# Performance work log

Hardware: AMD Instinct MI355X
Metric: run time of the kernel (lower is better)

The kernel has to match this reference:

```python
import jax, jax.numpy as jnp
import numpy as np

DIM = 1024
HEADS = 16
HEAD_DIM = DIM // HEADS


def setup_inputs() -> dict:
    key = jax.random.key(0)
    ks = jax.random.split(key, 5)
    B, N = 4, 2048
    x = jax.random.normal(ks[0], (B, N, DIM), dtype=jnp.float32)
    # nn.Linear default init scale ~ 1/sqrt(fan_in)
    s = 1.0 / np.sqrt(DIM)
    W_qkv = jax.random.uniform(ks[1], (DIM, 3 * DIM), minval=-s, maxval=s, dtype=jnp.float32)
    b_qkv = jax.random.uniform(ks[2], (3 * DIM,), minval=-s, maxval=s, dtype=jnp.float32)
    W_proj = jax.random.uniform(ks[3], (DIM, DIM), minval=-s, maxval=s, dtype=jnp.float32)
    b_proj = jax.random.uniform(ks[4], (DIM,), minval=-s, maxval=s, dtype=jnp.float32)
    return {"x": x, "W_qkv": W_qkv, "b_qkv": b_qkv, "W_proj": W_proj, "b_proj": b_proj}


def reference(x, W_qkv, b_qkv, W_proj, b_proj):
    B, N, C = x.shape
    qkv = x @ W_qkv + b_qkv                      # [B, N, 3C]
    qkv = qkv.reshape(B, N, 3, HEADS, HEAD_DIM)
    q = jnp.transpose(qkv[:, :, 0], (0, 2, 1, 3))  # [B, H, N, D]
    k = jnp.transpose(qkv[:, :, 1], (0, 2, 1, 3))
    v = jnp.transpose(qkv[:, :, 2], (0, 2, 1, 3))
    scale = 1.0 / np.sqrt(HEAD_DIM)
    scores = jnp.einsum('bhqd,bhkd->bhqk', q, k) * scale  # [B, H, N, N]
    attn = jax.nn.softmax(scores, axis=-1)
    out = jnp.einsum('bhqk,bhkd->bhqd', attn, v)           # [B, H, N, D]
    out = jnp.transpose(out, (0, 2, 1, 3)).reshape(B, N, C)
    return out @ W_proj + b_proj
```

## Files before the change

kernel.cpp:

```cpp
#include <hip/hip_runtime.h>

typedef __attribute__((ext_vector_type(4)))  float  f32x4;
typedef __attribute__((ext_vector_type(16))) float  f32x16;
typedef __attribute__((ext_vector_type(8)))  short  short8;
typedef __attribute__((ext_vector_type(4)))  unsigned int u32x4;
typedef __attribute__((ext_vector_type(2)))  unsigned int uint2v;

#define MFMA16 __builtin_amdgcn_mfma_f32_16x16x32_bf16
#define MFMA32 __builtin_amdgcn_mfma_f32_32x32x16_bf16

static __device__ __forceinline__ unsigned short f2bf(float f){
  union { float f; unsigned u; } v; v.f = f;
  unsigned r = v.u + 0x7fffu + ((v.u >> 16) & 1u);
  return (unsigned short)(r >> 16);
}

static __device__ __forceinline__ unsigned cvtpk(float a, float b){
  unsigned r;
  asm("v_cvt_pk_bf16_f32 %0, %1, %2" : "=v"(r) : "v"(a), "v"(b));
  return r;
}

typedef __attribute__((address_space(1))) void gvoid_t;
typedef __attribute__((address_space(3))) void lvoid_t;

static __device__ __forceinline__ void gll16(const unsigned short* g, unsigned short* l){
  __builtin_amdgcn_global_load_lds((gvoid_t*)g, (lvoid_t*)l, 16, 0, 0);
}


__global__ __launch_bounds__(256) void k_convert(const float* __restrict__ x,
                                                 unsigned short* __restrict__ xb){
  __shared__ __align__(16) unsigned short sm[16384];
  const int mblk = blockIdx.x >> 4, kt = blockIdx.x & 15;
  const int t = threadIdx.x;
  const int l16 = t & 15, rg = t >> 4;
  #pragma unroll
  for (int p = 0; p < 16; p++){
    int row = p * 16 + rg;
    f32x4 v = *(const f32x4*)&x[(size_t)(mblk*256 + row) * 1024 + kt*64 + l16*4];
    uint2v u; u[0] = cvtpk(v[0], v[1]); u[1] = cvtpk(v[2], v[3]);
    int g = l16 >> 1;
    *(uint2v*)&sm[row*64 + ((g ^ (row & 7)) << 3) + (l16 & 1)*4] = u;
  }
  __syncthreads();
  size_t obase = (size_t)((mblk*16 + kt)*2) * 8192;
  #pragma unroll
  for (int i = 0; i < 8; i++){
    int o = i * 256 + t;
    int kh = o >> 10, rem = o & 1023;
    int band = rem >> 6, cc = (rem >> 4) & 3, ri = rem & 15;
    int r = band*16 + ri, g = kh*4 + cc;
    short8 vv = *(const short8*)&sm[r*64 + ((g ^ (r & 7)) << 3)];
    *(short8*)&xb[obase + (size_t)kh*8192 + rem*8] = vv;
  }
}

__global__ __launch_bounds__(256) void k_transpose(const float* __restrict__ W,
                                                   unsigned short* __restrict__ Wt,
                                                   int K, int N){
  __shared__ float tile[32][33];
  int n0 = blockIdx.x * 32, k0 = blockIdx.y * 32;
  int tx = threadIdx.x, ty = threadIdx.y;
  #pragma unroll
  for (int r = 0; r < 4; r++)
    tile[ty + 8*r][tx] = W[(size_t)(k0 + ty + 8*r) * N + n0 + tx];
  __syncthreads();
  #pragma unroll
  for (int r = 0; r < 4; r++){
    int nn = ty + 8*r;
    int n = n0 + nn, k = k0 + tx;
    int kt = k >> 6, kh = (k >> 5) & 1, cc = (k >> 3) & 3, ke = k & 7;
    int nblk = n >> 8, band = (n & 255) >> 4, ri = n & 15;
    Wt[(size_t)(((nblk*16 + kt)*2 + kh)) * 8192 + band*512 + cc*128 + ri*8 + ke] =
        f2bf(tile[tx][nn]);
  }
}

#define GSYNC3 { __builtin_amdgcn_sched_barrier(0);                        \
                 asm volatile("s_waitcnt vmcnt(3)" ::: "memory");          \
                 __builtin_amdgcn_s_barrier();                             \
                 __builtin_amdgcn_sched_barrier(0); }
#define GSYNC0 { __builtin_amdgcn_sched_barrier(0);                        \
                 asm volatile("s_waitcnt vmcnt(0)" ::: "memory");          \
                 __builtin_amdgcn_s_barrier();                             \
                 __builtin_amdgcn_sched_barrier(0); }

template<int MODE>
__global__ __launch_bounds__(512, 2) void k_gemm(const unsigned short* __restrict__ A,
                                                 const unsigned short* __restrict__ Bt,
                                                 const float* __restrict__ bias,
                                                 void* __restrict__ outp,
                                                 int NT){
  __shared__ __align__(16) unsigned short lds[49152];
  const int t = threadIdx.x, w = t >> 6, l = t & 63;
  const int wr = w >> 2, wc = w & 3;
  const int bx = blockIdx.x, by = blockIdx.y;
  const int mblk = bx >> 1, mhalf = bx & 1;

  const unsigned short* Ab = A + (size_t)mblk*262144 + mhalf*4096 + t*8;
  const unsigned short* Bb = Bt + (size_t)by*262144 + t*8;

  f32x4 acc[4][4];
  #pragma unroll
  for (int i = 0; i < 4; i++)
    #pragma unroll
    for (int j = 0; j < 4; j++)
      acc[i][j] = (f32x4){0.f, 0.f, 0.f, 0.f};

#define GSTAGE(c2, ks, ktile) {                                                   \
    gll16(Ab + (size_t)(ktile)*16384 + (ks)*8192, &lds[(c2)*8192 + (ks)*4096 + t*8]); \
    gll16(Bb + (size_t)(ktile)*16384 + (ks)*8192, &lds[16384 + (c2)*16384 + (ks)*8192 + t*8]); \
    gll16(Bb + (size_t)(ktile)*16384 + (ks)*8192 + 4096, &lds[16384 + (c2)*16384 + (ks)*8192 + 4096 + t*8]); }

#define GPHASE(c2, ks) {                                                          \
    short8 af[4], bfr[4];                                                         \
    const int aoff = (c2)*8192 + (ks)*4096 + wr*2048 + l*8;                       \
    const int boff = 16384 + (c2)*16384 + (ks)*8192 + wc*2048 + l*8;              \
    _Pragma("unroll")                                                             \
    for (int i = 0; i < 4; i++) af[i]  = *(const short8*)&lds[aoff + i*512];      \
    _Pragma("unroll")                                                             \
    for (int j = 0; j < 4; j++) bfr[j] = *(const short8*)&lds[boff + j*512];      \
    __builtin_amdgcn_s_setprio(1);                                                \
    _Pragma("unroll")                                                             \
    for (int i = 0; i < 4; i++)                                                   \
      _Pragma("unroll")                                                           \
      for (int j = 0; j < 4; j++)                                                 \
        acc[i][j] = MFMA16(af[i], bfr[j], acc[i][j], 0, 0, 0);                    \
    __builtin_amdgcn_s_setprio(0); }

  GSTAGE(0, 0, 0);
  GSTAGE(0, 1, 0);
  GSYNC3;

  for (int kt2 = 0; kt2 < NT; kt2++){
    const int c = kt2 & 1, n2 = c ^ 1;
    const bool pre = kt2 < NT - 1;
    if (pre) GSTAGE(n2, 0, kt2 + 1);
    GPHASE(c, 0);
    if (pre) GSYNC3 else GSYNC0;
    if (pre) GSTAGE(n2, 1, kt2 + 1);
    GPHASE(c, 1);
    if (pre) GSYNC3;
  }

  if (MODE == 0){
    unsigned short* qg = (unsigned short*)outp;
    unsigned short* kg = qg + (size_t)8388608;
    unsigned short* vg = kg + (size_t)8388608;
    const int which = by >> 2;
    #pragma unroll
    for (int j = 0; j < 4; j++){
      int col = by*256 + wc*64 + j*16 + (l & 15);
      float bi = bias[col];
      int cc = col & 1023;
      int h = cc >> 6, d = cc & 63;
      if (which == 2){
        #pragma unroll
        for (int i = 0; i < 4; i++){
          int row = bx*128 + wr*64 + i*16 + (l >> 4)*4;
          int b = row >> 11, nn = row & 2047;
          int off = nn & 63;
          int off2 = (off & 7) | (((off >> 3) ^ (d & 7)) << 3);
          uint2v u;
          u[0] = cvtpk(acc[i][j][0] + bi, acc[i][j][1] + bi);
          u[1] = cvtpk(acc[i][j][2] + bi, acc[i][j][3] + bi);
          *(uint2v*)&vg[(size_t)(b*16 + h)*131072 + (size_t)d*2048 + (nn & ~63) + off2] = u;
        }
      } else {
        unsigned short* dst = which ? kg : qg;
        float scale = which ? 1.0f : 0.18033688011f;
        #pragma unroll
        for (int i = 0; i < 4; i++)
          #pragma unroll
          for (int reg = 0; reg < 4; reg++){
            int row = bx*128 + wr*64 + i*16 + (l >> 4)*4 + reg;
            int b = row >> 11, nn = row & 2047;
            int d2 = (d & 7) | (((d >> 3) ^ (nn & 7)) << 3);
            dst[(size_t)(b*16 + h)*131072 + (size_t)nn*64 + d2] =
                f2bf((acc[i][j][reg] + bi) * scale);
          }
      }
    }
  } else {
    float* out = (float*)outp;
    #pragma unroll
    for (int i = 0; i < 4; i++)
      #pragma unroll
      for (int reg = 0; reg < 4; reg++){
        int row = bx*128 + wr*64 + i*16 + (l >> 4)*4 + reg;
        #pragma unroll
        for (int j = 0; j < 4; j++){
          int col = by*256 + wc*64 + j*16 + (l & 15);
          out[(size_t)row * 1024 + col] = acc[i][j][reg] + bias[col];
        }
      }
  }
#undef GSTAGE
#undef GPHASE
}

__global__ __launch_bounds__(512) void k_attn(const unsigned short* __restrict__ Qg,
                                              const unsigned short* __restrict__ Kg,
                                              const unsigned short* __restrict__ Vg,
                                              unsigned short* __restrict__ aout){
  __shared__ __align__(16) unsigned short lds[16384];

  const int t = threadIdx.x, w = t >> 6, l = t & 63;
  const int hi = l >> 5, q = l & 31, l7 = l & 7;
  const int bh = blockIdx.y, q0 = blockIdx.x * 256;
  const unsigned short* Qp = Qg + (size_t)bh * 131072 + (size_t)q0 * 64;
  const unsigned short* Kp = Kg + (size_t)bh * 131072;
  const unsigned short* Vp = Vg + (size_t)bh * 131072;

  #pragma unroll
  for (int i = 0; i < 4; i++){
    int c = i * 512 + t;
    gll16(Qp + c * 8, &lds[c * 8]);
  }
  __syncthreads();
  short8 qf[4];
  {
    int qrow = w * 32 + q;
    #pragma unroll
    for (int ds = 0; ds < 4; ds++)
      qf[ds] = *(const short8*)&lds[qrow * 64 + (((2*ds + hi) ^ (qrow & 7)) << 3)];
  }
  __syncthreads();

  gll16(Kp + t * 8, &lds[t * 8]);
  gll16(Vp + (size_t)(t >> 3) * 2048 + (t & 7) * 8, &lds[4096 + t * 8]);
  __syncthreads();

  int koff[2][4], voff[4][2];
  #pragma unroll
  for (int kb = 0; kb < 2; kb++)
    #pragma unroll
    for (int ds = 0; ds < 4; ds++)
      koff[kb][ds] = (kb*32 + q) * 64 + (((2*ds + hi) ^ l7) << 3);
  #pragma unroll
  for (int ks = 0; ks < 4; ks++)
    #pragma unroll
    for (int db = 0; db < 2; db++)
      voff[ks][db] = 4096 + (db*32 + q) * 64 + (((2*ks + hi) ^ l7) << 3);

  f32x16 oacc0, oacc1;
  #pragma unroll
  for (int i = 0; i < 16; i++){ oacc0[i] = 0.f; oacc1[i] = 0.f; }
  float m = -1e30f, lsum = 0.f;

  for (int kt = 0; kt < 32; kt++){
    const int cb = (kt & 1) * 8192;
    if (kt < 31){
      const int nb = cb ^ 8192;
      gll16(Kp + (size_t)(kt + 1) * 4096 + t * 8, &lds[nb + t * 8]);
      gll16(Vp + (size_t)(t >> 3) * 2048 + (size_t)(kt + 1) * 64 + (t & 7) * 8,
            &lds[nb + 4096 + t * 8]);
    }

    f32x16 sA, sB;
    #pragma unroll
    for (int i = 0; i < 16; i++){ sA[i] = 0.f; sB[i] = 0.f; }
    __builtin_amdgcn_s_setprio(1);
    #pragma unroll
    for (int ds = 0; ds < 4; ds++){
      short8 kfA = *(const short8*)&lds[cb + koff[0][ds]];
      short8 kfB = *(const short8*)&lds[cb + koff[1][ds]];
      sA = MFMA32(kfA, qf[ds], sA, 0, 0, 0);
      sB = MFMA32(kfB, qf[ds], sB, 0, 0, 0);
    }
    __builtin_amdgcn_s_setprio(0);

    float mxA = fmaxf(
      fmaxf(fmaxf(fmaxf(sA[0],sA[1]),fmaxf(sA[2],sA[3])),
            fmaxf(fmaxf(sA[4],sA[5]),fmaxf(sA[6],sA[7]))),
      fmaxf(fmaxf(fmaxf(sA[8],sA[9]),fmaxf(sA[10],sA[11])),
            fmaxf(fmaxf(sA[12],sA[13]),fmaxf(sA[14],sA[15]))));
    float mxB = fmaxf(
      fmaxf(fmaxf(fmaxf(sB[0],sB[1]),fmaxf(sB[2],sB[3])),
            fmaxf(fmaxf(sB[4],sB[5]),fmaxf(sB[6],sB[7]))),
      fmaxf(fmaxf(fmaxf(sB[8],sB[9]),fmaxf(sB[10],sB[11])),
            fmaxf(fmaxf(sB[12],sB[13]),fmaxf(sB[14],sB[15]))));
    float mx = fmaxf(mxA, mxB);
    mx = fmaxf(mx, __shfl_xor(mx, 32));
    if (!__all(mx - m <= 8.0f)){
      float mn = fmaxf(m, mx);
      float sf = __builtin_amdgcn_exp2f(m - mn);
      m = mn; lsum *= sf;
      #pragma unroll
      for (int i = 0; i < 16; i++){ oacc0[i] *= sf; oacc1[i] *= sf; }
    }
    #pragma unroll
    for (int i = 0; i < 16; i++){
      sA[i] = __builtin_amdgcn_exp2f(sA[i] - m);
      sB[i] = __builtin_amdgcn_exp2f(sB[i] - m);
    }
    float rsA = (((sA[0]+sA[1])+(sA[2]+sA[3])) + ((sA[4]+sA[5])+(sA[6]+sA[7])))
              + (((sA[8]+sA[9])+(sA[10]+sA[11])) + ((sA[12]+sA[13])+(sA[14]+sA[15])));
    float rsB = (((sB[0]+sB[1])+(sB[2]+sB[3])) + ((sB[4]+sB[5])+(sB[6]+sB[7])))
              + (((sB[8]+sB[9])+(sB[10]+sB[11])) + ((sB[12]+sB[13])+(sB[14]+sB[15])));
    float rs = rsA + rsB;
    rs += __shfl_xor(rs, 32);
    lsum += rs;

    unsigned wA[8], wB[8];
    #pragma unroll
    for (int j = 0; j < 8; j++){
      wA[j] = cvtpk(sA[2*j], sA[2*j+1]);
      wB[j] = cvtpk(sB[2*j], sB[2*j+1]);
    }
    unsigned rA0 = __shfl_xor(hi ? wA[0] : wA[2], 32);
    unsigned rA1 = __shfl_xor(hi ? wA[1] : wA[3], 32);
    unsigned rA2 = __shfl_xor(hi ? wA[4] : wA[6], 32);
    unsigned rA3 = __shfl_xor(hi ? wA[5] : wA[7], 32);
    unsigned rB0 = __shfl_xor(hi ? wB[0] : wB[2], 32);
    unsigned rB1 = __shfl_xor(hi ? wB[1] : wB[3], 32);
    unsigned rB2 = __shfl_xor(hi ? wB[4] : wB[6], 32);
    unsigned rB3 = __shfl_xor(hi ? wB[5] : wB[7], 32);

    u32x4 pf[4];
    pf[0][0] = hi ? rA0 : wA[0]; pf[0][1] = hi ? rA1 : wA[1];
    pf[0][2] = hi ? wA[2] : rA0; pf[0][3] = hi ? wA[3] : rA1;
    pf[1][0] = hi ? rA2 : wA[4]; pf[1][1] = hi ? rA3 : wA[5];
    pf[1][2] = hi ? wA[6] : rA2; pf[1][3] = hi ? wA[7] : rA3;
    pf[2][0] = hi ? rB0 : wB[0]; pf[2][1] = hi ? rB1 : wB[1];
    pf[2][2] = hi ? wB[2] : rB0; pf[2][3] = hi ? wB[3] : rB1;
    pf[3][0] = hi ? rB2 : wB[4]; pf[3][1] = hi ? rB3 : wB[5];
    pf[3][2] = hi ? wB[6] : rB2; pf[3][3] = hi ? wB[7] : rB3;

    __builtin_amdgcn_s_setprio(1);
    #pragma unroll
    for (int ks = 0; ks < 4; ks++){
      short8 pfr;
      *(u32x4*)&pfr = pf[ks];
      short8 vf0 = *(const short8*)&lds[cb + voff[ks][0]];
      short8 vf1 = *(const short8*)&lds[cb + voff[ks][1]];
      oacc0 = MFMA32(vf0, pfr, oacc0, 0, 0, 0);
      oacc1 = MFMA32(vf1, pfr, oacc1, 0, 0, 0);
    }
    __builtin_amdgcn_s_setprio(0);

    __syncthreads();
  }

  {
    float inv = 1.0f / lsum;
    int qrow = w * 32 + q;
    #pragma unroll
    for (int j = 0; j < 8; j++){
      int d0 = 8*(j>>1) + 2*(j&1) + 4*hi;
      unsigned u0 = cvtpk(oacc0[2*j] * inv, oacc0[2*j+1] * inv);
      *(unsigned*)&lds[qrow*64 + (((d0>>3) ^ (qrow&7)) << 3) + (d0&7)] = u0;
      int d1 = d0 + 32;
      unsigned u1 = cvtpk(oacc1[2*j] * inv, oacc1[2*j+1] * inv);
      *(unsigned*)&lds[qrow*64 + (((d1>>3) ^ (qrow&7)) << 3) + (d1&7)] = u1;
    }
  }
  __syncthreads();
  {
    int mblk16 = (bh >> 4) * 8 + blockIdx.x;
    int h = bh & 15;
    size_t obase = (size_t)((mblk16*16 + h)*2) * 8192;
    #pragma unroll
    for (int i = 0; i < 4; i++){
      int idx = i * 512 + t;
      int kh = idx >> 10, rem = idx & 1023;
      int band = rem >> 6, cc = (rem >> 4) & 3, ri = rem & 15;
      int r = band*16 + ri, g = kh*4 + cc;
      short8 vv = *(const short8*)&lds[r*64 + ((g ^ (r & 7)) << 3)];
      *(short8*)&aout[obase + (size_t)kh*8192 + rem*8] = vv;
    }
  }
}

extern "C" void kernel_launch(void* const* d_in, const int* in_sizes, int n_in,
                              void* d_out, int out_size, void* d_ws, size_t ws_size,
                              hipStream_t stream){
  const float* x     = (const float*)d_in[0];
  const float* Wqkv  = (const float*)d_in[1];
  const float* bqkv  = (const float*)d_in[2];
  const float* Wproj = (const float*)d_in[3];
  const float* bproj = (const float*)d_in[4];

  unsigned short* ws   = (unsigned short*)d_ws;
  unsigned short* xb   = ws;
  unsigned short* Wqt  = ws + (size_t)8192 * 1024;
  unsigned short* Wpt  = Wqt + (size_t)3072 * 1024;
  unsigned short* qkvb = Wpt + (size_t)1024 * 1024;

  k_convert<<<512, 256, 0, stream>>>(x, xb);
  k_transpose<<<dim3(96, 32), dim3(32, 8), 0, stream>>>(Wqkv, Wqt, 1024, 3072);
  k_transpose<<<dim3(32, 32), dim3(32, 8), 0, stream>>>(Wproj, Wpt, 1024, 1024);
  k_gemm<0><<<dim3(64, 12), 512, 0, stream>>>(xb, Wqt, bqkv, qkvb, 16);
  k_attn<<<dim3(8, 64), 512, 0, stream>>>(qkvb, qkvb + (size_t)8388608,
                                          qkvb + (size_t)16777216, xb);
  k_gemm<1><<<dim3(64, 4), 512, 0, stream>>>(xb, Wpt, bproj, (void*)d_out, 16);
}
```

Before: 190.0 us.

## Pre-fragment Q/K/V layout for attention, smaller blocks with XCD-aware mapping

Result: no change. 188.3 us (-0.9%).

```diff
diff --git a/kernel.cpp b/kernel.cpp
--- a/kernel.cpp
+++ b/kernel.cpp
@@ -1,5 +1,6 @@
 #include <hip/hip_runtime.h>
 
+typedef __attribute__((ext_vector_type(2)))  float  f32x2;
 typedef __attribute__((ext_vector_type(4)))  float  f32x4;
 typedef __attribute__((ext_vector_type(16))) float  f32x16;
 typedef __attribute__((ext_vector_type(8)))  short  short8;
@@ -19,6 +20,14 @@
   unsigned r;
   asm("v_cvt_pk_bf16_f32 %0, %1, %2" : "=v"(r) : "v"(a), "v"(b));
   return r;
+}
+
+static __device__ __forceinline__ void plswap(unsigned &a, unsigned &b){
+  asm("v_permlane32_swap_b32 %0, %1" : "+v"(a), "+v"(b));
+}
+
+static __device__ __forceinline__ float max3f(float a, float b, float c){
+  return fmaxf(fmaxf(a, b), c);
 }
 
 typedef __attribute__((address_space(1))) void gvoid_t;
@@ -149,35 +158,38 @@
     unsigned short* kg = qg + (size_t)8388608;
     unsigned short* vg = kg + (size_t)8388608;
     const int which = by >> 2;
+    const int lrow = l & 15;
     #pragma unroll
     for (int j = 0; j < 4; j++){
-      int col = by*256 + wc*64 + j*16 + (l & 15);
+      int col = by*256 + wc*64 + j*16 + lrow;
       float bi = bias[col];
       int cc = col & 1023;
-      int h = cc >> 6, d = cc & 63;
+      int h = cc >> 6;
+      int d = j*16 + lrow;
       if (which == 2){
+        int db = d >> 5, dd = d & 31;
         #pragma unroll
         for (int i = 0; i < 4; i++){
-          int row = bx*128 + wr*64 + i*16 + (l >> 4)*4;
-          int b = row >> 11, nn = row & 2047;
-          int off = nn & 63;
-          int off2 = (off & 7) | (((off >> 3) ^ (d & 7)) << 3);
+          int nn = bx*128 + wr*64 + i*16 + (l >> 4)*4;
+          int b = nn >> 11, key = nn & 2047;
+          size_t idx = (size_t)(key >> 6)*4096 + (size_t)(((key >> 4) & 3)*2 + db)*512
+                     + (((key >> 3) & 1)*32 + dd)*8 + (key & 7);
           uint2v u;
           u[0] = cvtpk(acc[i][j][0] + bi, acc[i][j][1] + bi);
           u[1] = cvtpk(acc[i][j][2] + bi, acc[i][j][3] + bi);
-          *(uint2v*)&vg[(size_t)(b*16 + h)*131072 + (size_t)d*2048 + (nn & ~63) + off2] = u;
+          *(uint2v*)&vg[(size_t)(b*16 + h)*131072 + idx] = u;
         }
       } else {
         unsigned short* dst = which ? kg : qg;
         float scale = which ? 1.0f : 0.18033688011f;
+        int dsub = (d >> 4)*512 + ((d >> 3) & 1)*256 + (d & 7);
         #pragma unroll
         for (int i = 0; i < 4; i++)
           #pragma unroll
           for (int reg = 0; reg < 4; reg++){
-            int row = bx*128 + wr*64 + i*16 + (l >> 4)*4 + reg;
-            int b = row >> 11, nn = row & 2047;
-            int d2 = (d & 7) | (((d >> 3) ^ (nn & 7)) << 3);
-            dst[(size_t)(b*16 + h)*131072 + (size_t)nn*64 + d2] =
+            int nn = bx*128 + wr*64 + i*16 + (l >> 4)*4 + reg;
+            int b = nn >> 11, row = nn & 2047;
+            dst[(size_t)(b*16 + h)*131072 + (size_t)(row >> 5)*2048 + dsub + (row & 31)*8] =
                 f2bf((acc[i][j][reg] + bi) * scale);
           }
       }
@@ -200,49 +212,39 @@
 #undef GPHASE
 }
 
-__global__ __launch_bounds__(512) void k_attn(const unsigned short* __restrict__ Qg,
-                                              const unsigned short* __restrict__ Kg,
-                                              const unsigned short* __restrict__ Vg,
-                                              unsigned short* __restrict__ aout){
+__global__ __launch_bounds__(256, 4) void k_attn(const unsigned short* __restrict__ Qg,
+                                                 const unsigned short* __restrict__ Kg,
+                                                 const unsigned short* __restrict__ Vg,
+                                                 unsigned short* __restrict__ aout){
   __shared__ __align__(16) unsigned short lds[16384];
 
   const int t = threadIdx.x, w = t >> 6, l = t & 63;
-  const int hi = l >> 5, q = l & 31, l7 = l & 7;
-  const int bh = blockIdx.y, q0 = blockIdx.x * 256;
-  const unsigned short* Qp = Qg + (size_t)bh * 131072 + (size_t)q0 * 64;
-  const unsigned short* Kp = Kg + (size_t)bh * 131072;
-  const unsigned short* Vp = Vg + (size_t)bh * 131072;
-
-  #pragma unroll
-  for (int i = 0; i < 4; i++){
-    int c = i * 512 + t;
-    gll16(Qp + c * 8, &lds[c * 8]);
-  }
+  const int hi = l >> 5, q31 = l & 31;
+  const int d0 = blockIdx.x;
+  const int xcd = d0 & 7, jj = d0 >> 3;
+  const int bh = xcd + 8*(jj >> 4);
+  const int bx = jj & 15;
+
+  const unsigned short* Qp = Qg + (size_t)bh*131072 + (size_t)bx*8192;
+  const unsigned short* Kp = Kg + (size_t)bh*131072;
+  const unsigned short* Vp = Vg + (size_t)bh*131072;
+
+  #pragma unroll
+  for (int i = 0; i < 4; i++){ int c = i*256 + t; gll16(Qp + c*8, &lds[c*8]); }
   __syncthreads();
   short8 qf[4];
-  {
-    int qrow = w * 32 + q;
-    #pragma unroll
-    for (int ds = 0; ds < 4; ds++)
-      qf[ds] = *(const short8*)&lds[qrow * 64 + (((2*ds + hi) ^ (qrow & 7)) << 3)];
-  }
-  __syncthreads();
-
-  gll16(Kp + t * 8, &lds[t * 8]);
-  gll16(Vp + (size_t)(t >> 3) * 2048 + (t & 7) * 8, &lds[4096 + t * 8]);
-  __syncthreads();
-
-  int koff[2][4], voff[4][2];
-  #pragma unroll
-  for (int kb = 0; kb < 2; kb++)
-    #pragma unroll
-    for (int ds = 0; ds < 4; ds++)
-      koff[kb][ds] = (kb*32 + q) * 64 + (((2*ds + hi) ^ l7) << 3);
-  #pragma unroll
-  for (int ks = 0; ks < 4; ks++)
-    #pragma unroll
-    for (int db = 0; db < 2; db++)
-      voff[ks][db] = 4096 + (db*32 + q) * 64 + (((2*ks + hi) ^ l7) << 3);
+  #pragma unroll
+  for (int ds = 0; ds < 4; ds++)
+    qf[ds] = *(const short8*)&lds[(w*4 + ds)*512 + l*8];
+  __syncthreads();
+
+  #pragma unroll
+  for (int i = 0; i < 2; i++){
+    int c = i*256 + t;
+    gll16(Kp + c*8, &lds[c*8]);
+    gll16(Vp + c*8, &lds[4096 + c*8]);
+  }
+  __syncthreads();
 
   f32x16 oacc0, oacc1;
   #pragma unroll
@@ -253,9 +255,12 @@
     const int cb = (kt & 1) * 8192;
     if (kt < 31){
       const int nb = cb ^ 8192;
-      gll16(Kp + (size_t)(kt + 1) * 4096 + t * 8, &lds[nb + t * 8]);
-      gll16(Vp + (size_t)(t >> 3) * 2048 + (size_t)(kt + 1) * 64 + (t & 7) * 8,
-            &lds[nb + 4096 + t * 8]);
+      #pragma unroll
+      for (int i = 0; i < 2; i++){
+        int c = i*256 + t;
+        gll16(Kp + (size_t)(kt + 1)*4096 + c*8, &lds[nb + c*8]);
+        gll16(Vp + (size_t)(kt + 1)*4096 + c*8, &lds[nb + 4096 + c*8]);
+      }
     }
 
     f32x16 sA, sB;
@@ -264,24 +269,22 @@
     __builtin_amdgcn_s_setprio(1);
     #pragma unroll
     for (int ds = 0; ds < 4; ds++){
-      short8 kfA = *(const short8*)&lds[cb + koff[0][ds]];
-      short8 kfB = *(const short8*)&lds[cb + koff[1][ds]];
+      short8 kfA = *(const short8*)&lds[cb + ds*512 + l*8];
+      short8 kfB = *(const short8*)&lds[cb + 2048 + ds*512 + l*8];
       sA = MFMA32(kfA, qf[ds], sA, 0, 0, 0);
       sB = MFMA32(kfB, qf[ds], sB, 0, 0, 0);
     }
     __builtin_amdgcn_s_setprio(0);
 
-    float mxA = fmaxf(
-      fmaxf(fmaxf(fmaxf(sA[0],sA[1]),fmaxf(sA[2],sA[3])),
-            fmaxf(fmaxf(sA[4],sA[5]),fmaxf(sA[6],sA[7]))),
-      fmaxf(fmaxf(fmaxf(sA[8],sA[9]),fmaxf(sA[10],sA[11])),
-            fmaxf(fmaxf(sA[12],sA[13]),fmaxf(sA[14],sA[15]))));
-    float mxB = fmaxf(
-      fmaxf(fmaxf(fmaxf(sB[0],sB[1]),fmaxf(sB[2],sB[3])),
-            fmaxf(fmaxf(sB[4],sB[5]),fmaxf(sB[6],sB[7]))),
-      fmaxf(fmaxf(fmaxf(sB[8],sB[9]),fmaxf(sB[10],sB[11])),
-            fmaxf(fmaxf(sB[12],sB[13]),fmaxf(sB[14],sB[15]))));
-    float mx = fmaxf(mxA, mxB);
+    float mx = max3f(
+        max3f(max3f(sA[0], sA[1], sA[2]),  max3f(sA[3], sA[4], sA[5]),
+              max3f(sA[6], sA[7], sA[8])),
+        max3f(max3f(sA[9], sA[10], sA[11]), max3f(sA[12], sA[13], sA[14]),
+              max3f(sA[15], sB[0], sB[1])),
+        max3f(max3f(max3f(sB[2], sB[3], sB[4]),  max3f(sB[5], sB[6], sB[7]),
+                    max3f(sB[8], sB[9], sB[10])),
+              max3f(sB[11], sB[12], sB[13]),
+              fmaxf(sB[14], sB[15])));
     mx = fmaxf(mx, __shfl_xor(mx, 32));
     if (!__all(mx - m <= 8.0f)){
       float mn = fmaxf(m, mx);
@@ -290,51 +293,51 @@
       #pragma unroll
       for (int i = 0; i < 16; i++){ oacc0[i] *= sf; oacc1[i] *= sf; }
     }
-    #pragma unroll
-    for (int i = 0; i < 16; i++){
-      sA[i] = __builtin_amdgcn_exp2f(sA[i] - m);
-      sB[i] = __builtin_amdgcn_exp2f(sB[i] - m);
-    }
-    float rsA = (((sA[0]+sA[1])+(sA[2]+sA[3])) + ((sA[4]+sA[5])+(sA[6]+sA[7])))
-              + (((sA[8]+sA[9])+(sA[10]+sA[11])) + ((sA[12]+sA[13])+(sA[14]+sA[15])));
-    float rsB = (((sB[0]+sB[1])+(sB[2]+sB[3])) + ((sB[4]+sB[5])+(sB[6]+sB[7])))
-              + (((sB[8]+sB[9])+(sB[10]+sB[11])) + ((sB[12]+sB[13])+(sB[14]+sB[15])));
-    float rs = rsA + rsB;
+    f32x2 mm; mm[0] = m; mm[1] = m;
+    f32x2 a2[8], b2[8];
+    #pragma unroll
+    for (int j = 0; j < 8; j++){
+      f32x2 ta; ta[0] = sA[2*j]; ta[1] = sA[2*j+1];
+      f32x2 tb; tb[0] = sB[2*j]; tb[1] = sB[2*j+1];
+      a2[j] = ta - mm;
+      b2[j] = tb - mm;
+    }
+    #pragma unroll
+    for (int j = 0; j < 8; j++){
+      a2[j][0] = __builtin_amdgcn_exp2f(a2[j][0]);
+      a2[j][1] = __builtin_amdgcn_exp2f(a2[j][1]);
+      b2[j][0] = __builtin_amdgcn_exp2f(b2[j][0]);
+      b2[j][1] = __builtin_amdgcn_exp2f(b2[j][1]);
+    }
+    f32x2 s2 = ((a2[0] + a2[1]) + (a2[2] + a2[3])) + ((a2[4] + a2[5]) + (a2[6] + a2[7]))
+             + ((b2[0] + b2[1]) + (b2[2] + b2[3])) + ((b2[4] + b2[5]) + (b2[6] + b2[7]));
+    float rs = s2[0] + s2[1];
     rs += __shfl_xor(rs, 32);
     lsum += rs;
 
     unsigned wA[8], wB[8];
     #pragma unroll
     for (int j = 0; j < 8; j++){
-      wA[j] = cvtpk(sA[2*j], sA[2*j+1]);
-      wB[j] = cvtpk(sB[2*j], sB[2*j+1]);
-    }
-    unsigned rA0 = __shfl_xor(hi ? wA[0] : wA[2], 32);
-    unsigned rA1 = __shfl_xor(hi ? wA[1] : wA[3], 32);
-    unsigned rA2 = __shfl_xor(hi ? wA[4] : wA[6], 32);
-    unsigned rA3 = __shfl_xor(hi ? wA[5] : wA[7], 32);
-    unsigned rB0 = __shfl_xor(hi ? wB[0] : wB[2], 32);
-    unsigned rB1 = __shfl_xor(hi ? wB[1] : wB[3], 32);
-    unsigned rB2 = __shfl_xor(hi ? wB[4] : wB[6], 32);
-    unsigned rB3 = __shfl_xor(hi ? wB[5] : wB[7], 32);
-
+      wA[j] = cvtpk(a2[j][0], a2[j][1]);
+      wB[j] = cvtpk(b2[j][0], b2[j][1]);
+    }
     u32x4 pf[4];
-    pf[0][0] = hi ? rA0 : wA[0]; pf[0][1] = hi ? rA1 : wA[1];
-    pf[0][2] = hi ? wA[2] : rA0; pf[0][3] = hi ? wA[3] : rA1;
-    pf[1][0] = hi ? rA2 : wA[4]; pf[1][1] = hi ? rA3 : wA[5];
-    pf[1][2] = hi ? wA[6] : rA2; pf[1][3] = hi ? wA[7] : rA3;
-    pf[2][0] = hi ? rB0 : wB[0]; pf[2][1] = hi ? rB1 : wB[1];
-    pf[2][2] = hi ? wB[2] : rB0; pf[2][3] = hi ? wB[3] : rB1;
-    pf[3][0] = hi ? rB2 : wB[4]; pf[3][1] = hi ? rB3 : wB[5];
-    pf[3][2] = hi ? wB[6] : rB2; pf[3][3] = hi ? wB[7] : rB3;
+    { unsigned a = wA[0], b = wA[2]; plswap(a, b); pf[0][0] = a; pf[0][2] = b; }
+    { unsigned a = wA[1], b = wA[3]; plswap(a, b); pf[0][1] = a; pf[0][3] = b; }
+    { unsigned a = wA[4], b = wA[6]; plswap(a, b); pf[1][0] = a; pf[1][2] = b; }
+    { unsigned a = wA[5], b = wA[7]; plswap(a, b); pf[1][1] = a; pf[1][3] = b; }
+    { unsigned a = wB[0], b = wB[2]; plswap(a, b); pf[2][0] = a; pf[2][2] = b; }
+    { unsigned a = wB[1], b = wB[3]; plswap(a, b); pf[2][1] = a; pf[2][3] = b; }
+    { unsigned a = wB[4], b = wB[6]; plswap(a, b); pf[3][0] = a; pf[3][2] = b; }
+    { unsigned a = wB[5], b = wB[7]; plswap(a, b); pf[3][1] = a; pf[3][3] = b; }
 
     __builtin_amdgcn_s_setprio(1);
     #pragma unroll
     for (int ks = 0; ks < 4; ks++){
       short8 pfr;
       *(u32x4*)&pfr = pf[ks];
-      short8 vf0 = *(const short8*)&lds[cb + voff[ks][0]];
-      short8 vf1 = *(const short8*)&lds[cb + voff[ks][1]];
+      short8 vf0 = *(const short8*)&lds[cb + 4096 + (ks*2 + 0)*512 + l*8];
+      short8 vf1 = *(const short8*)&lds[cb + 4096 + (ks*2 + 1)*512 + l*8];
       oacc0 = MFMA32(vf0, pfr, oacc0, 0, 0, 0);
       oacc1 = MFMA32(vf1, pfr, oacc1, 0, 0, 0);
     }
@@ -345,30 +348,30 @@
 
   {
     float inv = 1.0f / lsum;
-    int qrow = w * 32 + q;
+    int qrow = w*32 + q31;
     #pragma unroll
     for (int j = 0; j < 8; j++){
-      int d0 = 8*(j>>1) + 2*(j&1) + 4*hi;
+      int dd0 = 8*(j >> 1) + 2*(j & 1) + 4*hi;
       unsigned u0 = cvtpk(oacc0[2*j] * inv, oacc0[2*j+1] * inv);
-      *(unsigned*)&lds[qrow*64 + (((d0>>3) ^ (qrow&7)) << 3) + (d0&7)] = u0;
-      int d1 = d0 + 32;
+      *(unsigned*)&lds[qrow*64 + (((dd0 >> 3) ^ (qrow & 7)) << 3) + (dd0 & 7)] = u0;
+      int dd1 = dd0 + 32;
       unsigned u1 = cvtpk(oacc1[2*j] * inv, oacc1[2*j+1] * inv);
-      *(unsigned*)&lds[qrow*64 + (((d1>>3) ^ (qrow&7)) << 3) + (d1&7)] = u1;
+      *(unsigned*)&lds[qrow*64 + (((dd1 >> 3) ^ (qrow & 7)) << 3) + (dd1 & 7)] = u1;
     }
   }
   __syncthreads();
   {
-    int mblk16 = (bh >> 4) * 8 + blockIdx.x;
+    int mblk16 = (bh >> 4)*8 + (bx >> 1);
     int h = bh & 15;
-    size_t obase = (size_t)((mblk16*16 + h)*2) * 8192;
+    int bandbase = 8*(bx & 1);
     #pragma unroll
     for (int i = 0; i < 4; i++){
-      int idx = i * 512 + t;
-      int kh = idx >> 10, rem = idx & 1023;
-      int band = rem >> 6, cc = (rem >> 4) & 3, ri = rem & 15;
-      int r = band*16 + ri, g = kh*4 + cc;
+      int idx = i*256 + t;
+      int kh = idx >> 9, band_l = (idx >> 6) & 7, cc = (idx >> 4) & 3, ri = idx & 15;
+      int r = band_l*16 + ri, g = kh*4 + cc;
       short8 vv = *(const short8*)&lds[r*64 + ((g ^ (r & 7)) << 3)];
-      *(short8*)&aout[obase + (size_t)kh*8192 + rem*8] = vv;
+      size_t chunk = (size_t)((mblk16*16 + h)*2 + kh);
+      *(short8*)&aout[chunk*8192 + (size_t)(bandbase + band_l)*512 + cc*128 + ri*8] = vv;
     }
   }
 }
@@ -392,7 +395,7 @@
   k_transpose<<<dim3(96, 32), dim3(32, 8), 0, stream>>>(Wqkv, Wqt, 1024, 3072);
   k_transpose<<<dim3(32, 32), dim3(32, 8), 0, stream>>>(Wproj, Wpt, 1024, 1024);
   k_gemm<0><<<dim3(64, 12), 512, 0, stream>>>(xb, Wqt, bqkv, qkvb, 16);
-  k_attn<<<dim3(8, 64), 512, 0, stream>>>(qkvb, qkvb + (size_t)8388608,
-                                          qkvb + (size_t)16777216, xb);
+  k_attn<<<1024, 256, 0, stream>>>(qkvb, qkvb + (size_t)8388608,
+                                   qkvb + (size_t)16777216, xb);
   k_gemm<1><<<dim3(64, 4), 512, 0, stream>>>(xb, Wpt, bproj, (void*)d_out, 16);
 }
```
